# Kernel optimization log

Hardware: AMD Instinct MI355X
Metric: run time of the kernel (lower is better)

## Reference

```python
import jax, jax.numpy as jnp
import numpy as np

HIDDEN = 512
EMBED = 512
VOCAB = 32000
BRANCH = 4
LEVELS = 9  # level 0 = root, level LEVELS-1 = leaves (complete 4-ary tree)
N_NODES = sum(BRANCH ** l for l in range(LEVELS))  # 87381


def setup_inputs() -> dict:
    key = jax.random.key(0)
    ks = jax.random.split(key, 16)
    s = 1.0 / np.sqrt(HIDDEN)
    inp = {
        "token_ids": jax.random.randint(ks[0], (N_NODES,), 0, VOCAB, dtype=jnp.int32),
        "emb": jax.random.normal(ks[1], (VOCAB, EMBED), jnp.float32) * 0.02,
        "Wi": jax.random.normal(ks[2], (EMBED, HIDDEN), jnp.float32) * s,
        "Ui": jax.random.normal(ks[3], (HIDDEN, HIDDEN), jnp.float32) * s,
        "bi": jnp.zeros((HIDDEN,), jnp.float32),
        "Wf": jax.random.normal(ks[4], (EMBED, HIDDEN), jnp.float32) * s,
        "Uf": jax.random.normal(ks[5], (HIDDEN, HIDDEN), jnp.float32) * s,
        "bf": jnp.zeros((HIDDEN,), jnp.float32),
        "Wo": jax.random.normal(ks[6], (EMBED, HIDDEN), jnp.float32) * s,
        "Uo": jax.random.normal(ks[7], (HIDDEN, HIDDEN), jnp.float32) * s,
        "bo": jnp.zeros((HIDDEN,), jnp.float32),
        "Wu": jax.random.normal(ks[8], (EMBED, HIDDEN), jnp.float32) * s,
        "Uu": jax.random.normal(ks[9], (HIDDEN, HIDDEN), jnp.float32) * s,
        "bu": jnp.zeros((HIDDEN,), jnp.float32),
        "branching": BRANCH,
        "n_levels": LEVELS,
    }
    return inp


def reference(token_ids, emb, Wi, Ui, bi, Wf, Uf, bf, Wo, Uo, bo, Wu, Uu, bu,
              branching, n_levels):
    # Level-synchronous Child-Sum Tree-LSTM over a complete `branching`-ary tree.
    # token_ids is laid out level by level, root first.
    B = int(branching)
    L = int(n_levels)
    H = Wi.shape[1]
    level_sizes = [B ** l for l in range(L)]
    offsets = np.concatenate([[0], np.cumsum(level_sizes)])  # static Python ints

    # Leaves: original code sets h = c = 0 (leaf embedding is computed but unused).
    h = jnp.zeros((level_sizes[-1], H), dtype=emb.dtype)
    c = jnp.zeros((level_sizes[-1], H), dtype=emb.dtype)
    hs_levels = [h]  # hidden states collected leaves -> root (level order)

    for l in range(L - 2, -1, -1):
        n = level_sizes[l]
        x = jnp.take(emb, token_ids[offsets[l]:offsets[l + 1]], axis=0)  # [n, E]
        ch_h = h.reshape(n, B, H)  # children of node k are contiguous
        ch_c = c.reshape(n, B, H)
        h_tilde = ch_h.sum(axis=1)  # [n, H] child-sum
        i = jax.nn.sigmoid(x @ Wi + h_tilde @ Ui + bi)
        # per-child forget gates: [n, B, H]
        f = jax.nn.sigmoid((x @ Wf + bf)[:, None, :] + ch_h @ Uf)
        o = jax.nn.sigmoid(x @ Wo + h_tilde @ Uo + bo)
        u = jnp.tanh(x @ Wu + h_tilde @ Uu + bu)
        c = i * u + (f * ch_c).sum(axis=1)
        h = o * jnp.tanh(c)
        hs_levels.append(h)

    hidden_states = jnp.concatenate(hs_levels, axis=0)  # [N_NODES, H]
    return hidden_states, h, c  # h, c are the root states, shape [1, H]
```

## Files before the change

### kernel.cpp

```cpp
#include <hip/hip_runtime.h>

#define DI __device__ __forceinline__

typedef __attribute__((ext_vector_type(8))) __bf16 bf16x8;
typedef __attribute__((ext_vector_type(4))) float f32x4;
typedef __attribute__((ext_vector_type(8))) unsigned short ushort8;
typedef unsigned long long ull;

static DI unsigned short f2b(float f) {
  unsigned int x = __builtin_bit_cast(unsigned int, f);
  unsigned int r = (x + 0x7FFFu + ((x >> 16) & 1u)) >> 16;
  return (unsigned short)r;
}
static DI float b2f(unsigned short u) {
  return __builtin_bit_cast(float, (unsigned int)u << 16);
}
static DI float sigmf(float x) { return 1.0f / (1.0f + __expf(-x)); }

typedef const __attribute__((address_space(1))) void* gcptr;
typedef __attribute__((address_space(3))) void* lptr;
static DI void gl_lds16(const void* g, void* l) {
  __builtin_amdgcn_global_load_lds((gcptr)g, (lptr)l, 16, 0, 0);
}

#define GCOL(g, d) ((((d) >> 4) << 6) + ((g) << 4) + ((d) & 15))

static DI size_t qaddr(int NT, int row4, int c) {
  int tm = row4 >> 5, tn = c >> 7;
  int rq = row4 & 31, c7 = c & 127;
  int wv = ((rq >> 4) << 1) | (c7 >> 6);
  int mf = (rq >> 2) & 3, nf = (c7 >> 4) & 3;
  int lane = ((rq & 3) << 4) | (c7 & 15);
  return ((size_t)(tm * NT + tn) << 12) + (size_t)((((wv << 4) + (mf << 2) + nf) << 6) + lane);
}

__global__ void prep_pack(const float* __restrict__ Wi, const float* __restrict__ Ui,
                          const float* __restrict__ bi, const float* __restrict__ Wf,
                          const float* __restrict__ Uf, const float* __restrict__ bfv,
                          const float* __restrict__ Wo, const float* __restrict__ Uo,
                          const float* __restrict__ bo, const float* __restrict__ Wu,
                          const float* __restrict__ Uu, const float* __restrict__ bu,
                          unsigned short* __restrict__ Wp, unsigned short* __restrict__ Upiou,
                          unsigned short* __restrict__ Upf, float* __restrict__ bias)
{
  int u = blockIdx.x * blockDim.x + threadIdx.x;
  if (u < 131072) {
    int k8 = u >> 11, n = u & 2047;
    int gate = (n >> 4) & 3;
    int d = ((n >> 6) << 4) | (n & 15);
    const float* W = (gate == 0) ? Wi : (gate == 1) ? Wf : (gate == 2) ? Wo : Wu;
    ushort8 pk;
    #pragma unroll
    for (int t = 0; t < 8; ++t) pk[t] = f2b(W[(size_t)(k8*8+t)*512 + d]);
    *(ushort8*)&Wp[(size_t)u*8] = pk;
  } else if (u < 131072 + 98304) {
    int v = u - 131072;
    int k8 = v / 1536, n = v - k8*1536;
    const float* U = (n < 512) ? Ui : (n < 1024) ? Uo : Uu;
    int c = n & 511;
    ushort8 pk;
    #pragma unroll
    for (int t = 0; t < 8; ++t) pk[t] = f2b(U[(size_t)(k8*8+t)*512 + c]);
    *(ushort8*)&Upiou[(size_t)v*8] = pk;
  } else {
    int v = u - 229376;
    int k8 = v >> 9, c = v & 511;
    ushort8 pk;
    #pragma unroll
    for (int t = 0; t < 8; ++t) pk[t] = f2b(Uf[(size_t)(k8*8+t)*512 + c]);
    *(ushort8*)&Upf[(size_t)v*8] = pk;
  }
  if (u < 2048) {
    int gate = (u >> 4) & 3;
    int d = ((u >> 6) << 4) | (u & 15);
    bias[u] = (gate == 0) ? bi[d] : (gate == 1) ? bfv[d] : (gate == 2) ? bo[d] : bu[d];
  }
}

__global__ void gather_x(const int* __restrict__ tok, const float* __restrict__ emb,
                         unsigned short* __restrict__ X)
{
  int u = blockIdx.x * blockDim.x + threadIdx.x;
  if (u >= 22272*64) return;
  int R = u >> 6, ch = u & 63;
  int l, node;
  if (R < 512)       { l = R >> 7; node = R & 127; int sz = 1 << (2*l); if (node >= sz) node = sz - 1; }
  else if (R < 768)  { l = 4; node = R - 512; }
  else if (R < 1792) { l = 5; node = R - 768; }
  else if (R < 5888) { l = 6; node = R - 1792; }
  else               { l = 7; node = R - 5888; }
  static const int offs_c[8] = {0,1,5,21,85,341,1365,5461};
  int tk = tok[offs_c[l] + node];
  const float* src = emb + (size_t)tk*512 + ch*8;
  ushort8 pk;
  #pragma unroll
  for (int t = 0; t < 8; ++t) pk[t] = f2b(src[t]);
  *(ushort8*)&X[(size_t)u*8] = pk;
}

struct GDesc {
  const unsigned short* A;
  const unsigned short* Bp;
  ull* C;
  int M, N, NT;
};
struct L7P {
  float* hout; unsigned short* hb; float* cb; unsigned short* ht;
};

template<bool FUSED>
__global__ __launch_bounds__(256)
void gemm512(GDesc g1, GDesc g2, int split, const float* __restrict__ bias, L7P l7,
             float* __restrict__ zbase, size_t z4)
{
  __shared__ unsigned short As[2*128*64];
  __shared__ unsigned short Bs[2*8*128*8];

  const int nwg = gridDim.x, orig = blockIdx.x;
  const int q = nwg >> 3, r = nwg & 7;
  const int xcd = orig & 7, idx = orig >> 3;
  const int wg = (xcd < r ? xcd*(q+1) : r*(q+1) + (xcd-r)*q) + idx;

  const bool role1 = (wg < split);
  GDesc g = role1 ? g1 : g2;
  const int lwg = role1 ? wg : wg - split;
  const int tm = lwg / g.NT, tn = lwg - tm * g.NT;

  const int tid = threadIdx.x;
  const int wave = tid >> 6, lane = tid & 63;
  const int Mbase = tm * 128, Nbase = tn * 128;
  const int wr = wave >> 1, wc = wave & 1;
  const int l15 = lane & 15, l4 = lane >> 4;

  const int arow_l = wave*8 + (lane >> 3);
  const int acol8  = lane & 7;
  const int sw8    = arow_l & 7;

  f32x4 acc[4][4] = {};

  auto STAGE = [&](int p, int k0) {
    #pragma unroll
    for (int c = 0; c < 4; ++c) {
      int grow = Mbase + c*32 + arow_l;
      if (grow >= g.M) grow = g.M - 1;
      gl_lds16(g.A + (size_t)grow*512 + k0 + ((acol8 ^ sw8) * 8),
               As + p*(128*64) + (c*32 + wave*8)*64);
    }
    #pragma unroll
    for (int c = 0; c < 4; ++c) {
      int k8 = c*2 + (wave >> 1);
      int colh = (wave & 1) * 64;
      gl_lds16(g.Bp + ((size_t)((k0 >> 3) + k8) * g.N + Nbase + colh + lane) * 8,
               Bs + p*(8*128*8) + (k8*128 + colh)*8);
    }
  };

  auto COMPUTE = [&](int p) {
    #pragma unroll
    for (int ks = 0; ks < 2; ++ks) {
      bf16x8 af[4], bfr[4];
      #pragma unroll
      for (int mf = 0; mf < 4; ++mf) {
        int row = wr*64 + mf*16 + l15;
        int kc  = ks*4 + l4;
        af[mf] = *(const bf16x8*)&As[p*(128*64) + row*64 + ((kc ^ (row & 7)) * 8)];
      }
      #pragma unroll
      for (int nf = 0; nf < 4; ++nf) {
        int col = wc*64 + nf*16 + l15;
        int k8  = ks*4 + l4;
        bfr[nf] = *(const bf16x8*)&Bs[p*(8*128*8) + (k8*128 + col) * 8];
      }
      #pragma unroll
      for (int mf = 0; mf < 4; ++mf)
        #pragma unroll
        for (int nf = 0; nf < 4; ++nf)
          acc[mf][nf] = __builtin_amdgcn_mfma_f32_16x16x32_bf16(af[mf], bfr[nf], acc[mf][nf], 0, 0, 0);
    }
  };

  STAGE(0, 0);
  __syncthreads();
  #pragma unroll
  for (int it = 0; it < 7; ++it) {
    STAGE((it + 1) & 1, (it + 1) * 64);
    COMPUTE(it & 1);
    __syncthreads();
  }
  COMPUTE(1);

  if (FUSED && tm >= 46) {
    const float bi_ = bias[Nbase + wc*64      + l15];
    const float bo_ = bias[Nbase + wc*64 + 32 + l15];
    const float bu_ = bias[Nbase + wc*64 + 48 + l15];
    const int d = tn*32 + wc*16 + l15;
    #pragma unroll
    for (int mf = 0; mf < 4; ++mf) {
      int node0 = Mbase - 5888 + wr*64 + mf*16 + l4*4;
      float hts = 0.f;
      #pragma unroll
      for (int rr = 0; rr < 4; ++rr) {
        float iv = sigmf(acc[mf][0][rr] + bi_);
        float ov = sigmf(acc[mf][2][rr] + bo_);
        float uv = tanhf(acc[mf][3][rr] + bu_);
        float cv = iv * uv;
        float hv = ov * tanhf(cv);
        size_t node = node0 + rr;
        l7.hout[node*512 + d] = hv;
        l7.hb[node*512 + d]   = f2b(hv);
        l7.cb[node*512 + d]   = cv;
        hts += hv;
      }
      l7.ht[(size_t)(node0 >> 2)*512 + d] = f2b(hts);
    }
  } else {
    float bv[4];
    #pragma unroll
    for (int nf = 0; nf < 4; ++nf)
      bv[nf] = (bias != nullptr && role1) ? bias[Nbase + wc*64 + nf*16 + l15] : 0.f;
    ull* Cb = g.C + ((size_t)(tm * g.NT + tn) << 12) + ((size_t)wave << 10);
    #pragma unroll
    for (int mf = 0; mf < 4; ++mf)
      #pragma unroll
      for (int nf = 0; nf < 4; ++nf) {
        f32x4 a = acc[mf][nf];
        ull pk = (ull)f2b(a[0] + bv[nf]) | ((ull)f2b(a[1] + bv[nf]) << 16)
               | ((ull)f2b(a[2] + bv[nf]) << 32) | ((ull)f2b(a[3] + bv[nf]) << 48);
        Cb[(mf*4 + nf)*64 + lane] = pk;
      }
  }

  if (zbase != nullptr) {
    f32x4 z = {0.f, 0.f, 0.f, 0.f};
    f32x4* zp = (f32x4*)zbase;
    size_t stride = (size_t)nwg * 256;
    for (size_t off = (size_t)orig*256 + tid; off < z4; off += stride) zp[off] = z;
  }
}

static DI void tile_gemm(const unsigned short* __restrict__ A, int M,
                         const unsigned short* __restrict__ Bp, int N, int NT,
                         int tm, int tn, ull* __restrict__ C, int wave, int lane)
{
  const int wr = wave >> 1, wc = wave & 1;
  const int l15 = lane & 15, l4 = lane >> 4;
  size_t a0[4]; unsigned int b0[4];
  #pragma unroll
  for (int mf = 0; mf < 4; ++mf) {
    int row = tm*128 + wr*64 + mf*16 + l15;
    if (row >= M) row = M - 1;
    a0[mf] = (size_t)row*512 + l4*8;
  }
  #pragma unroll
  for (int nf = 0; nf < 4; ++nf)
    b0[nf] = (unsigned int)(((unsigned)l4 * N + tn*128 + wc*64 + nf*16 + l15) * 8);
  const unsigned int bstep = (unsigned int)N * 32;

  f32x4 acc[4][4] = {};
  #pragma unroll
  for (int ks = 0; ks < 16; ++ks) {
    bf16x8 af[4], bfr[4];
    #pragma unroll
    for (int mf = 0; mf < 4; ++mf) af[mf] = *(const bf16x8*)(A + a0[mf] + ks*32);
    #pragma unroll
    for (int nf = 0; nf < 4; ++nf) bfr[nf] = *(const bf16x8*)(Bp + b0[nf] + ks*bstep);
    #pragma unroll
    for (int mf = 0; mf < 4; ++mf)
      #pragma unroll
      for (int nf = 0; nf < 4; ++nf)
        acc[mf][nf] = __builtin_amdgcn_mfma_f32_16x16x32_bf16(af[mf], bfr[nf], acc[mf][nf], 0, 0, 0);
  }
  ull* Cb = C + ((size_t)(tm * NT + tn) << 12) + ((size_t)wave << 10);
  #pragma unroll
  for (int mf = 0; mf < 4; ++mf)
    #pragma unroll
    for (int nf = 0; nf < 4; ++nf) {
      f32x4 a = acc[mf][nf];
      ull pk = (ull)f2b(a[0]) | ((ull)f2b(a[1]) << 16)
             | ((ull)f2b(a[2]) << 32) | ((ull)f2b(a[3]) << 48);
      Cb[(mf*4 + nf)*64 + lane] = pk;
    }
}

__global__ __launch_bounds__(256)
void gemm_small(GDesc g1, GDesc g2, int split)
{
  const int b = blockIdx.x;
  const bool role1 = (b < split);
  GDesc g = role1 ? g1 : g2;
  const int lb = role1 ? b : b - split;
  tile_gemm(g.A, g.M, g.Bp, g.N, g.NT, lb / g.NT, lb % g.NT, g.C,
            threadIdx.x >> 6, threadIdx.x & 63);
}

__global__ __launch_bounds__(256)
void combine2(const ull* __restrict__ Gq, const ull* __restrict__ Rq,
              const ull* __restrict__ Fq, const float* __restrict__ cch,
              float* __restrict__ hout, unsigned short* __restrict__ hbf,
              float* __restrict__ cout, unsigned short* __restrict__ htout,
              float* __restrict__ rootx, int n)
{
  const int b = blockIdx.x, t = threadIdx.x;
  #pragma unroll
  for (int half = 0; half < 2; ++half) {
    const int c = t + half * 256;
    ull gi4 = Gq[qaddr(16, b, GCOL(0, c))];
    ull gf4 = Gq[qaddr(16, b, GCOL(1, c))];
    ull go4 = Gq[qaddr(16, b, GCOL(2, c))];
    ull gu4 = Gq[qaddr(16, b, GCOL(3, c))];
    ull ri4 = Rq[qaddr(12, b, c)];
    ull ro4 = Rq[qaddr(12, b, c + 512)];
    ull ru4 = Rq[qaddr(12, b, c + 1024)];
    float hts = 0.f;
    #pragma unroll
    for (int rI = 0; rI < 4; ++rI) {
      int j = b*4 + rI;
      float gi = b2f((unsigned short)(gi4 >> (16*rI)));
      float gf = b2f((unsigned short)(gf4 >> (16*rI)));
      float go = b2f((unsigned short)(go4 >> (16*rI)));
      float gu = b2f((unsigned short)(gu4 >> (16*rI)));
      float iv = sigmf(gi + b2f((unsigned short)(ri4 >> (16*rI))));
      float ov = sigmf(go + b2f((unsigned short)(ro4 >> (16*rI))));
      float uv = tanhf(gu + b2f((unsigned short)(ru4 >> (16*rI))));
      ull f4 = Fq[qaddr(4, j, c)];
      const float* cc = cch + (size_t)(j*4)*512 + c;
      float fs = 0.f;
      #pragma unroll
      for (int k = 0; k < 4; ++k)
        fs += sigmf(gf + b2f((unsigned short)(f4 >> (16*k)))) * cc[(size_t)k*512];
      float cv = iv*uv + fs;
      float hv = ov * tanhf(cv);
      if (j < n) {
        hout[(size_t)j*512 + c] = hv;
        hbf[(size_t)j*512 + c]  = f2b(hv);
        cout[(size_t)j*512 + c] = cv;
        if (rootx && j == 0) { rootx[c] = hv; rootx[512 + c] = cv; }
        hts += hv;
      }
    }
    if (htout) htout[(size_t)b*512 + c] = f2b(hts);
  }
}

extern "C" void kernel_launch(void* const* d_in, const int* in_sizes, int n_in,
                              void* d_out, int out_size, void* d_ws, size_t ws_size,
                              hipStream_t stream)
{
  const int*   tok = (const int*)d_in[0];
  const float* emb = (const float*)d_in[1];
  const float* Wi  = (const float*)d_in[2];
  const float* Ui  = (const float*)d_in[3];
  const float* bi  = (const float*)d_in[4];
  const float* Wf  = (const float*)d_in[5];
  const float* Uf  = (const float*)d_in[6];
  const float* bfv = (const float*)d_in[7];
  const float* Wo  = (const float*)d_in[8];
  const float* Uo  = (const float*)d_in[9];
  const float* bo  = (const float*)d_in[10];
  const float* Wu  = (const float*)d_in[11];
  const float* Uu  = (const float*)d_in[12];
  const float* bu  = (const float*)d_in[13];

  char* ws = (char*)d_ws;
  unsigned short* Wp    = (unsigned short*)(ws + 0);
  unsigned short* Upiou = (unsigned short*)(ws + 2097152);
  unsigned short* Upf   = (unsigned short*)(ws + 3670016);
  float*          bias  = (float*)        (ws + 4194304);
  unsigned short* hbf   = (unsigned short*)(ws + 4202752);
  unsigned short* htbf  = (unsigned short*)(ws + 26572032);
  float*          cbuf  = (float*)        (ws + 32164096);
  ull*            RiouQ = (ull*)          (ws + 76902656);
  ull*            RfQ   = (ull*)          (ws + 89485568);
  ull*            Gq    = (ull*)          (ws + 106262784);
  unsigned short* X     = (unsigned short*)(ws + 130380032);

  float* fout = (float*)d_out;

  static const int  offs[9]    = {0,1,5,21,85,341,1365,5461,21845};
  static const int  padbase[8] = {0,128,256,384,512,768,1792,5888};
  static const long outoff[8]  = {87380,87376,87360,87296,87040,86016,81920,65536};

  prep_pack<<<1024, 256, 0, stream>>>(Wi,Ui,bi,Wf,Uf,bfv,Wo,Uo,bo,Wu,Uu,bu,
                                      Wp,Upiou,Upf,bias);
  gather_x<<<(22272*64)/256, 256, 0, stream>>>(tok, emb, X);

  GDesc gA { X, Wp, Gq, 22272, 2048, 16 };
  L7P l7 { fout + (size_t)outoff[7]*512, hbf + (size_t)offs[7]*512,
           cbuf + (size_t)offs[7]*512, htbf + (size_t)offs[6]*512 };
  gemm512<true><<<174*16, 256, 0, stream>>>(gA, gA, 174*16, bias, l7, nullptr, 0);

  L7P l7n {};
  {
    GDesc g1 { htbf + (size_t)offs[6]*512, Upiou, RiouQ, 4096,  1536, 12 };
    GDesc g2 { hbf  + (size_t)offs[7]*512, Upf,   RfQ,   16384, 512,  4  };
    gemm512<false><<<32*12 + 128*4, 256, 0, stream>>>(g1, g2, 32*12, nullptr, l7n,
                                                      fout, (size_t)65536*512/4);
    combine2<<<1024, 256, 0, stream>>>(
        Gq + (size_t)padbase[6]*512, RiouQ, RfQ, cbuf + (size_t)offs[7]*512,
        fout + (size_t)outoff[6]*512, hbf + (size_t)offs[6]*512, cbuf + (size_t)offs[6]*512,
        htbf + (size_t)offs[5]*512, nullptr, 4096);
  }
  {
    GDesc g1 { htbf + (size_t)offs[5]*512, Upiou, RiouQ, 1024, 1536, 12 };
    GDesc g2 { hbf  + (size_t)offs[6]*512, Upf,   RfQ,   4096, 512,  4  };
    gemm512<false><<<8*12 + 32*4, 256, 0, stream>>>(g1, g2, 8*12, nullptr, l7n, nullptr, 0);
    combine2<<<256, 256, 0, stream>>>(
        Gq + (size_t)padbase[5]*512, RiouQ, RfQ, cbuf + (size_t)offs[6]*512,
        fout + (size_t)outoff[5]*512, hbf + (size_t)offs[5]*512, cbuf + (size_t)offs[5]*512,
        htbf + (size_t)offs[4]*512, nullptr, 1024);
  }
  for (int l = 4; l >= 0; --l) {
    int n = 1 << (2*l);
    int t1 = ((n + 127) >> 7) * 12;
    int t2 = ((4*n + 127) >> 7) * 4;
    GDesc g1 { htbf + (size_t)offs[l]*512,   Upiou, RiouQ, n,   1536, 12 };
    GDesc g2 { hbf  + (size_t)offs[l+1]*512, Upf,   RfQ,   4*n, 512,  4  };
    gemm_small<<<t1 + t2, 256, 0, stream>>>(g1, g2, t1);
    combine2<<<(n + 3) / 4, 256, 0, stream>>>(
        Gq + (size_t)padbase[l]*512, RiouQ, RfQ, cbuf + (size_t)offs[l+1]*512,
        fout + (size_t)outoff[l]*512, hbf + (size_t)offs[l]*512, cbuf + (size_t)offs[l]*512,
        (l > 0) ? htbf + (size_t)offs[l-1]*512 : nullptr,
        (l == 0) ? fout + (size_t)87381*512 : nullptr,
        n);
  }
}
```

Baseline: 295.5 us.

## Fuse top three tree levels into one kernel; load B fragments directly from global

```diff
diff --git a/kernel.cpp b/kernel.cpp
--- a/kernel.cpp
+++ b/kernel.cpp
@@ -109,12 +109,11 @@
 };
 
 template<bool FUSED>
-__global__ __launch_bounds__(256)
+__global__ __launch_bounds__(256, 4)
 void gemm512(GDesc g1, GDesc g2, int split, const float* __restrict__ bias, L7P l7,
              float* __restrict__ zbase, size_t z4)
 {
   __shared__ unsigned short As[2*128*64];
-  __shared__ unsigned short Bs[2*8*128*8];
 
   const int nwg = gridDim.x, orig = blockIdx.x;
   const int q = nwg >> 3, r = nwg & 7;
@@ -146,19 +145,16 @@
       gl_lds16(g.A + (size_t)grow*512 + k0 + ((acol8 ^ sw8) * 8),
                As + p*(128*64) + (c*32 + wave*8)*64);
     }
-    #pragma unroll
-    for (int c = 0; c < 4; ++c) {
-      int k8 = c*2 + (wave >> 1);
-      int colh = (wave & 1) * 64;
-      gl_lds16(g.Bp + ((size_t)((k0 >> 3) + k8) * g.N + Nbase + colh + lane) * 8,
-               Bs + p*(8*128*8) + (k8*128 + colh)*8);
-    }
   };
 
-  auto COMPUTE = [&](int p) {
+  auto COMPUTE = [&](int p, int k0) {
     #pragma unroll
     for (int ks = 0; ks < 2; ++ks) {
       bf16x8 af[4], bfr[4];
+      #pragma unroll
+      for (int nf = 0; nf < 4; ++nf)
+        bfr[nf] = *(const bf16x8*)(g.Bp +
+            ((size_t)((k0 >> 3) + ks*4 + l4) * g.N + Nbase + wc*64 + nf*16 + l15) * 8);
       #pragma unroll
       for (int mf = 0; mf < 4; ++mf) {
         int row = wr*64 + mf*16 + l15;
@@ -166,12 +162,6 @@
         af[mf] = *(const bf16x8*)&As[p*(128*64) + row*64 + ((kc ^ (row & 7)) * 8)];
       }
       #pragma unroll
-      for (int nf = 0; nf < 4; ++nf) {
-        int col = wc*64 + nf*16 + l15;
-        int k8  = ks*4 + l4;
-        bfr[nf] = *(const bf16x8*)&Bs[p*(8*128*8) + (k8*128 + col) * 8];
-      }
-      #pragma unroll
       for (int mf = 0; mf < 4; ++mf)
         #pragma unroll
         for (int nf = 0; nf < 4; ++nf)
@@ -184,10 +174,10 @@
   #pragma unroll
   for (int it = 0; it < 7; ++it) {
     STAGE((it + 1) & 1, (it + 1) * 64);
-    COMPUTE(it & 1);
+    COMPUTE(it & 1, it * 64);
     __syncthreads();
   }
-  COMPUTE(1);
+  COMPUTE(1, 448);
 
   if (FUSED && tm >= 46) {
     const float bi_ = bias[Nbase + wc*64      + l15];
@@ -293,14 +283,11 @@
             threadIdx.x >> 6, threadIdx.x & 63);
 }
 
-__global__ __launch_bounds__(256)
-void combine2(const ull* __restrict__ Gq, const ull* __restrict__ Rq,
-              const ull* __restrict__ Fq, const float* __restrict__ cch,
-              float* __restrict__ hout, unsigned short* __restrict__ hbf,
-              float* __restrict__ cout, unsigned short* __restrict__ htout,
-              float* __restrict__ rootx, int n)
-{
-  const int b = blockIdx.x, t = threadIdx.x;
+static DI void combine_body(const ull* Gq, const ull* Rq, const ull* Fq,
+                            const float* cch, float* hout, unsigned short* hbf,
+                            float* cout, unsigned short* htout, float* rootx,
+                            int n, int b, int t)
+{
   #pragma unroll
   for (int half = 0; half < 2; ++half) {
     const int c = t + half * 256;
@@ -339,6 +326,69 @@
       }
     }
     if (htout) htout[(size_t)b*512 + c] = f2b(hts);
+  }
+}
+
+__global__ __launch_bounds__(256)
+void combine2(const ull* Gq, const ull* Rq, const ull* Fq, const float* cch,
+              float* hout, unsigned short* hbf, float* cout,
+              unsigned short* htout, float* rootx, int n)
+{
+  combine_body(Gq, Rq, Fq, cch, hout, hbf, cout, htout, rootx, n,
+               blockIdx.x, threadIdx.x);
+}
+
+__global__ __launch_bounds__(256)
+void tail(unsigned short* hbf, unsigned short* htbf, float* cbuf,
+          const unsigned short* Upiou, const unsigned short* Upf,
+          ull* RiouQ, ull* RfQ, const ull* Gq, float* fout)
+{
+  static const int offs_c[9]   = {0,1,5,21,85,341,1365,5461,21845};
+  static const int padbase_c[8]= {0,128,256,384,512,768,1792,5888};
+  static const int outoff_c[8] = {87380,87376,87360,87296,87040,86016,81920,65536};
+  const int t = threadIdx.x, wave = t >> 6, lane = t & 63;
+  const int l15 = lane & 15, l4 = lane >> 4;
+
+  for (int l = 2; l >= 0; --l) {
+    const int n = 1 << (2*l);
+    const int T1 = ((n + 15) >> 4) * 96;
+    const int T2 = ((4*n + 15) >> 4) * 32;
+    for (int tt = wave; tt < T1 + T2; tt += 4) {
+      const unsigned short* A; const unsigned short* Bp; ull* C;
+      int M, N, NT, tm16, tn16;
+      if (tt < T1) {
+        A = htbf + (size_t)offs_c[l]*512; M = n; Bp = Upiou; N = 1536; NT = 12;
+        tm16 = tt / 96; tn16 = tt - tm16*96; C = RiouQ;
+      } else {
+        int u = tt - T1;
+        A = hbf + (size_t)offs_c[l+1]*512; M = 4*n; Bp = Upf; N = 512; NT = 4;
+        tm16 = u / 32; tn16 = u - tm16*32; C = RfQ;
+      }
+      int row = tm16*16 + l15; if (row >= M) row = M - 1;
+      int col = tn16*16 + l15;
+      f32x4 acc = {0.f, 0.f, 0.f, 0.f};
+      #pragma unroll
+      for (int m = 0; m < 16; ++m) {
+        bf16x8 af = *(const bf16x8*)(A + (size_t)row*512 + (m*4 + l4)*8);
+        bf16x8 bf_ = *(const bf16x8*)(Bp + ((size_t)(m*4 + l4)*N + col)*8);
+        acc = __builtin_amdgcn_mfma_f32_16x16x32_bf16(af, bf_, acc, 0, 0, 0);
+      }
+      ull pk = (ull)f2b(acc[0]) | ((ull)f2b(acc[1]) << 16)
+             | ((ull)f2b(acc[2]) << 32) | ((ull)f2b(acc[3]) << 48);
+      C[qaddr(NT, tm16*4 + l4, col)] = pk;
+    }
+    __syncthreads();
+    const int groups = (n + 3) >> 2;
+    for (int b = 0; b < groups; ++b)
+      combine_body(Gq + (size_t)padbase_c[l]*512, RiouQ, RfQ,
+                   cbuf + (size_t)offs_c[l+1]*512,
+                   fout + (size_t)outoff_c[l]*512,
+                   hbf + (size_t)offs_c[l]*512,
+                   cbuf + (size_t)offs_c[l]*512,
+                   (l > 0) ? htbf + (size_t)offs_c[l-1]*512 : nullptr,
+                   (l == 0) ? fout + (size_t)87381*512 : nullptr,
+                   n, b, t);
+    __syncthreads();
   }
 }
 
@@ -409,7 +459,7 @@
         fout + (size_t)outoff[5]*512, hbf + (size_t)offs[5]*512, cbuf + (size_t)offs[5]*512,
         htbf + (size_t)offs[4]*512, nullptr, 1024);
   }
-  for (int l = 4; l >= 0; --l) {
+  for (int l = 4; l >= 3; --l) {
     int n = 1 << (2*l);
     int t1 = ((n + 127) >> 7) * 12;
     int t2 = ((4*n + 127) >> 7) * 4;
@@ -419,8 +469,7 @@
     combine2<<<(n + 3) / 4, 256, 0, stream>>>(
         Gq + (size_t)padbase[l]*512, RiouQ, RfQ, cbuf + (size_t)offs[l+1]*512,
         fout + (size_t)outoff[l]*512, hbf + (size_t)offs[l]*512, cbuf + (size_t)offs[l]*512,
-        (l > 0) ? htbf + (size_t)offs[l-1]*512 : nullptr,
-        (l == 0) ? fout + (size_t)87381*512 : nullptr,
-        n);
-  }
-}
+        htbf + (size_t)offs[l-1]*512, nullptr, n);
+  }
+  tail<<<1, 256, 0, stream>>>(hbf, htbf, cbuf, Upiou, Upf, RiouQ, RfQ, Gq, fout);
+}
```

New measurement: 605.0 us. +104.7%, slower.
